# Kernel tuning notes

Hardware: AMD Instinct MI355X
Metric: run time of the kernel (lower is better)

Reference implementation:

```python
import jax, jax.numpy as jnp
import numpy as np

DATA_DIM = 8
NOISE_DIM = 8
HIDDEN = 128
N_STEPS = 100
BATCH = 65536


def _mlp3(tx, w1, b1, w2, b2, w3, b3):
    h = jnp.tanh(tx @ w1 + b1)
    h = jnp.tanh(h @ w2 + b2)
    return h @ w3 + b3


def setup_inputs() -> dict:
    key = jax.random.key(0)
    ks = jax.random.split(key, 20)
    s = 0.05
    d, nd, h = DATA_DIM, NOISE_DIM, HIDDEN
    inp = {
        "x": jax.random.normal(ks[0], (BATCH, d), jnp.float32),
        "initial_noise": jax.random.normal(ks[1], (BATCH, nd), jnp.float32),
        "dW": jax.random.normal(ks[2], (N_STEPS - 1, BATCH, nd), jnp.float32),
        # drift MLP: (1+d) -> h -> h -> d
        "drift_w1": jax.random.normal(ks[3], (1 + d, h), jnp.float32) * s,
        "drift_b1": jnp.zeros((h,), jnp.float32),
        "drift_w2": jax.random.normal(ks[4], (h, h), jnp.float32) * s,
        "drift_b2": jnp.zeros((h,), jnp.float32),
        "drift_w3": jax.random.normal(ks[5], (h, d), jnp.float32) * s,
        "drift_b3": jnp.zeros((d,), jnp.float32),
        # diffusion MLP: (1+d) -> h -> h -> d*nd
        "diff_w1": jax.random.normal(ks[6], (1 + d, h), jnp.float32) * s,
        "diff_b1": jnp.zeros((h,), jnp.float32),
        "diff_w2": jax.random.normal(ks[7], (h, h), jnp.float32) * s,
        "diff_b2": jnp.zeros((h,), jnp.float32),
        "diff_w3": jax.random.normal(ks[8], (h, d * nd), jnp.float32) * s,
        "diff_b3": jnp.zeros((d * nd,), jnp.float32),
        # initial-condition MLP: nd -> h -> d (num_layers=2)
        "init_w1": jax.random.normal(ks[9], (nd, h), jnp.float32) * s,
        "init_b1": jnp.zeros((h,), jnp.float32),
        "init_w2": jax.random.normal(ks[10], (h, d), jnp.float32) * s,
        "init_b2": jnp.zeros((d,), jnp.float32),
    }
    return inp


def reference(x, initial_noise, dW,
              drift_w1, drift_b1, drift_w2, drift_b2, drift_w3, drift_b3,
              diff_w1, diff_b1, diff_w2, diff_b2, diff_w3, diff_b3,
              init_w1, init_b1, init_w2, init_b2):
    batch = x.shape[0]
    n_steps = dW.shape[0] + 1
    dt = 1.0 / (n_steps - 1)
    sqrt_dt = jnp.sqrt(jnp.float32(dt))
    t_span = jnp.linspace(0.0, 1.0, n_steps, dtype=x.dtype)

    # initial condition: initial_net(noise)
    x0 = jnp.tanh(initial_noise @ init_w1 + init_b1) @ init_w2 + init_b2  # [B, d]

    def step(xc, inputs):
        t, dWi = inputs  # t scalar, dWi [B, nd]
        tcol = jnp.full((batch, 1), t, dtype=xc.dtype)
        tx = jnp.concatenate([tcol, xc], axis=1)  # [B, 1+d]
        f = _mlp3(tx, drift_w1, drift_b1, drift_w2, drift_b2, drift_w3, drift_b3)  # [B, d]
        g = _mlp3(tx, diff_w1, diff_b1, diff_w2, diff_b2, diff_w3, diff_b3)
        g = g.reshape(batch, DATA_DIM, NOISE_DIM)  # [B, d, nd]
        # Euler-Maruyama update: dx = f*dt + g @ (dW*sqrt(dt))
        dx = f * dt + jnp.einsum('bdn,bn->bd', g, dWi * sqrt_dt)
        xn = xc + dx
        return xn, xn

    _, xs = jax.lax.scan(step, x0, (t_span[:-1], dW))  # xs: [T-1, B, d]
    path = jnp.concatenate([x0[None], xs], axis=0)  # [T, B, d]
    path = jnp.transpose(path, (1, 0, 2))  # [B, T, d]
    return path.reshape(batch, -1)  # data_dim > 1 branch of forward
```

## Files before the change

### kernel.cpp

```cpp
#include <hip/hip_runtime.h>

typedef short bf16x8 __attribute__((ext_vector_type(8)));
typedef float f32x16 __attribute__((ext_vector_type(16)));
typedef unsigned int u32;
typedef unsigned int u32x4 __attribute__((ext_vector_type(4)));

#define NB 65536
#define STR2 136
#define STR1 24
#define OFF_W1  0
#define OFF_W2D 6144
#define OFF_W2F 23552
#define OFF_W3D 40960
#define OFF_W3F 45312
#define LDS_SHORTS 54016

__device__ __forceinline__ u32 bfr(float f) {
    u32 u = __builtin_bit_cast(u32, f);
    return (u + 0x7fffu + ((u >> 16) & 1u)) >> 16;
}
__device__ __forceinline__ u32 pkbf16(float a, float b) {
    return bfr(a) | (bfr(b) << 16);
}
__device__ __forceinline__ short bf16s(float a) {
    return (short)bfr(a);
}
__device__ __forceinline__ float ftanh(float x) {
    float e = __expf(2.0f * x);
    float r = __builtin_amdgcn_rcpf(e + 1.0f);
    return __builtin_fmaf(-2.0f, r, 1.0f);
}
__device__ __forceinline__ bf16x8 fragU(u32 a, u32 b, u32 c, u32 d) {
    u32x4 q = {a, b, c, d};
    return __builtin_bit_cast(bf16x8, q);
}
__device__ __forceinline__ bf16x8 fragV(u32x4 q) {
    return __builtin_bit_cast(bf16x8, q);
}
__device__ __forceinline__ bf16x8 ldsfrag(const short* p) {
    const u32x4* q = (const u32x4*)p;
    return __builtin_bit_cast(bf16x8, *q);
}
__device__ __forceinline__ f32x16 mf(bf16x8 a, bf16x8 b, f32x16 c) {
    return __builtin_amdgcn_mfma_f32_32x32x16_bf16(a, b, c, 0, 0, 0);
}

struct F2 { u32x4 a, b; };
__device__ __forceinline__ F2 transition(const f32x16 d, int hi) {
    u32 P[8], Q[8];
    #pragma unroll
    for (int i = 0; i < 8; ++i)
        P[i] = pkbf16(ftanh(d[2*i]), ftanh(d[2*i+1]));
    #pragma unroll
    for (int i = 0; i < 8; ++i)
        Q[i] = __shfl_xor(P[i], 32, 64);
    F2 r;
    r.a[0] = hi ? Q[2] : P[0];   r.a[1] = hi ? Q[3] : P[1];
    r.a[2] = hi ? P[2] : Q[0];   r.a[3] = hi ? P[3] : Q[1];
    r.b[0] = hi ? Q[6] : P[4];   r.b[1] = hi ? Q[7] : P[5];
    r.b[2] = hi ? P[6] : Q[4];   r.b[3] = hi ? P[7] : Q[5];
    return r;
}

__global__ __launch_bounds__(512, 2)
void sde_fused(const float* __restrict__ noise, const float* __restrict__ dW,
               const float* __restrict__ dw1, const float* __restrict__ db1,
               const float* __restrict__ dw2, const float* __restrict__ db2,
               const float* __restrict__ dw3, const float* __restrict__ db3,
               const float* __restrict__ fw1, const float* __restrict__ fb1,
               const float* __restrict__ fw2, const float* __restrict__ fb2,
               const float* __restrict__ fw3, const float* __restrict__ fb3,
               const float* __restrict__ iw1, const float* __restrict__ ib1,
               const float* __restrict__ iw2, const float* __restrict__ ib2,
               float* __restrict__ out)
{
    extern __shared__ short lds[];
    const int tid  = threadIdx.x;
    const int lane = tid & 63;
    const int col  = lane & 31;
    const int hi   = lane >> 5;
    const int wid  = tid >> 6;
    const int row  = blockIdx.x * 256 + wid * 32 + col;

    for (int idx = tid; idx < LDS_SHORTS; idx += 512) lds[idx] = 0;
    __syncthreads();
    for (int idx = tid; idx < 128*128; idx += 512) {
        int k = idx >> 7, m = idx & 127;
        lds[OFF_W2D + m*STR2 + k] = bf16s(dw2[idx]);
        lds[OFF_W2F + m*STR2 + k] = bf16s(fw2[idx]);
    }
    for (int idx = tid; idx < 128*64; idx += 512) {
        int k = idx >> 6, m = idx & 63;
        lds[OFF_W3F + m*STR2 + k] = bf16s(fw3[idx]);
    }
    for (int idx = tid; idx < 128*8; idx += 512) {
        int k = idx >> 3, m = idx & 7;
        lds[OFF_W3D + m*STR2 + k] = bf16s(dw3[idx]);
    }
    for (int idx = tid; idx < 9*128; idx += 512) {
        int k = idx >> 7, m = idx & 127;
        lds[OFF_W1 + m*STR1 + k]       = bf16s(dw1[idx]);
        lds[OFF_W1 + (m+128)*STR1 + k] = bf16s(fw1[idx]);
    }
    if (tid < 128) {
        lds[OFF_W1 + tid*STR1 + 9]       = bf16s(db1[tid]);
        lds[OFF_W1 + (tid+128)*STR1 + 9] = bf16s(fb1[tid]);
    }

    const bf16x8 BB = fragU(hi ? 0u : 0x3F80u, 0u, 0u, 0u);

    float x[8];
    {
        const float4 n0 = *(const float4*)(noise + (size_t)row*8);
        const float4 n1 = *(const float4*)(noise + (size_t)row*8 + 4);
        bf16x8 Bi = fragU(hi ? pkbf16(1.f,0.f) : pkbf16(n0.x,n0.y),
                          hi ? 0u : pkbf16(n0.z,n0.w),
                          hi ? 0u : pkbf16(n1.x,n1.y),
                          hi ? 0u : pkbf16(n1.z,n1.w));
        u32x4 Hf[8];
        #pragma unroll
        for (int mt = 0; mt < 4; ++mt) {
            int m = mt*32 + col;
            float wv[8];
            #pragma unroll
            for (int j = 0; j < 8; ++j) {
                int k = hi*8 + j;
                float v = 0.f;
                if (k < 8) v = iw1[(size_t)k*128 + m];
                else if (k == 8) v = ib1[m];
                wv[j] = v;
            }
            bf16x8 A = fragU(pkbf16(wv[0],wv[1]), pkbf16(wv[2],wv[3]),
                             pkbf16(wv[4],wv[5]), pkbf16(wv[6],wv[7]));
            f32x16 dacc = {};
            dacc = mf(A, Bi, dacc);
            F2 t = transition(dacc, hi);
            Hf[2*mt] = t.a; Hf[2*mt+1] = t.b;
        }
        f32x16 dx0 = {};
        #pragma unroll
        for (int kt = 0; kt < 8; ++kt) {
            float wv[8];
            #pragma unroll
            for (int j = 0; j < 8; ++j) {
                int k = kt*16 + hi*8 + j;
                wv[j] = (col < 8) ? iw2[(size_t)k*8 + col] : 0.f;
            }
            bf16x8 A = fragU(pkbf16(wv[0],wv[1]), pkbf16(wv[2],wv[3]),
                             pkbf16(wv[4],wv[5]), pkbf16(wv[6],wv[7]));
            dx0 = mf(A, fragV(Hf[kt]), dx0);
        }
        u32 ba = (!hi && col < 8) ? pkbf16(ib2[col], 0.f) : 0u;
        dx0 = mf(fragU(ba,0u,0u,0u), BB, dx0);
        #pragma unroll
        for (int r = 0; r < 4; ++r) {
            float cv  = dx0[r];
            float clo = hi ? 0.f : cv;
            float chi = hi ? cv  : 0.f;
            x[r]   = clo + __shfl_xor(clo, 32, 64);
            x[r+4] = chi + __shfl_xor(chi, 32, 64);
        }
    }

    u32 ba2d[4], ba2f[4], ba3f[2], ba3d;
    #pragma unroll
    for (int mt = 0; mt < 4; ++mt) {
        ba2d[mt] = hi ? 0u : pkbf16(db2[mt*32+col], 0.f);
        ba2f[mt] = hi ? 0u : pkbf16(fb2[mt*32+col], 0.f);
    }
    ba3f[0] = hi ? 0u : pkbf16(fb3[col], 0.f);
    ba3f[1] = hi ? 0u : pkbf16(fb3[32+col], 0.f);
    ba3d    = (!hi && col < 8) ? pkbf16(db3[col], 0.f) : 0u;

    __syncthreads();

    const short* pW1  = lds + OFF_W1  + col*STR1 + hi*8;
    const short* pW2d = lds + OFF_W2D + col*STR2 + hi*8;
    const short* pW2f = lds + OFF_W2F + col*STR2 + hi*8;
    const short* pW3d = lds + OFF_W3D + col*STR2 + hi*8;
    const short* pW3f = lds + OFF_W3F + col*STR2 + hi*8;

    const float dtv  = 1.0f / 99.0f;
    const float sqdt = sqrtf(dtv);
    const float* dwp = dW + (size_t)row*8 + hi*4;
    float* outr = out + (size_t)row*800;

    float xp[8];
    #pragma unroll
    for (int d = 0; d < 8; ++d) xp[d] = x[d];

    #pragma unroll 1
    for (int st = 0; st < 99; ++st) {
        const float tv = (float)st * dtv;
        const float4 dv = *(const float4*)(dwp + (size_t)st * (NB*8));

        u32 c0 = hi ? pkbf16(x[7], 1.0f) : pkbf16(tv, x[0]);
        u32 c1 = hi ? 0u : pkbf16(x[1], x[2]);
        u32 c2 = hi ? 0u : pkbf16(x[3], x[4]);
        u32 c3 = hi ? 0u : pkbf16(x[5], x[6]);
        bf16x8 B1 = fragU(c0, c1, c2, c3);

        u32x4 B2[8], B3[8];
        #pragma unroll
        for (int mt = 0; mt < 4; ++mt) {
            f32x16 dacc = {};
            dacc = mf(ldsfrag(pW1 + mt*32*STR1), B1, dacc);
            F2 t = transition(dacc, hi);
            B2[2*mt] = t.a; B2[2*mt+1] = t.b;
        }
        #pragma unroll
        for (int mt = 0; mt < 4; ++mt) {
            f32x16 dacc = {};
            #pragma unroll
            for (int kt = 0; kt < 8; ++kt)
                dacc = mf(ldsfrag(pW2d + mt*32*STR2 + kt*16), fragV(B2[kt]), dacc);
            dacc = mf(fragU(ba2d[mt],0u,0u,0u), BB, dacc);
            F2 t = transition(dacc, hi);
            B3[2*mt] = t.a; B3[2*mt+1] = t.b;
        }
        f32x16 fa = {};
        #pragma unroll
        for (int kt = 0; kt < 8; ++kt)
            fa = mf(ldsfrag(pW3d + kt*16), fragV(B3[kt]), fa);
        fa = mf(fragU(ba3d,0u,0u,0u), BB, fa);
        const float f0 = fa[0], f1 = fa[1], f2 = fa[2], f3 = fa[3];

        #pragma unroll
        for (int mt = 0; mt < 4; ++mt) {
            f32x16 dacc = {};
            dacc = mf(ldsfrag(pW1 + (mt+4)*32*STR1), B1, dacc);
            F2 t = transition(dacc, hi);
            B2[2*mt] = t.a; B2[2*mt+1] = t.b;
        }
        #pragma unroll
        for (int mt = 0; mt < 4; ++mt) {
            f32x16 dacc = {};
            #pragma unroll
            for (int kt = 0; kt < 8; ++kt)
                dacc = mf(ldsfrag(pW2f + mt*32*STR2 + kt*16), fragV(B2[kt]), dacc);
            dacc = mf(fragU(ba2f[mt],0u,0u,0u), BB, dacc);
            F2 t = transition(dacc, hi);
            B3[2*mt] = t.a; B3[2*mt+1] = t.b;
        }

        float p[8] = {0.f,0.f,0.f,0.f,0.f,0.f,0.f,0.f};
        const float dws[4] = {dv.x*sqdt, dv.y*sqdt, dv.z*sqdt, dv.w*sqdt};
        #pragma unroll
        for (int gt = 0; gt < 2; ++gt) {
            f32x16 g = {};
            #pragma unroll
            for (int kt = 0; kt < 8; ++kt)
                g = mf(ldsfrag(pW3f + gt*32*STR2 + kt*16), fragV(B3[kt]), g);
            g = mf(fragU(ba3f[gt],0u,0u,0u), BB, g);
            #pragma unroll
            for (int r = 0; r < 16; ++r)
                p[gt*4 + (r>>2)] += g[r] * dws[r&3];
        }

        #pragma unroll
        for (int r = 0; r < 4; ++r) {
            float fv = (r==0?f0:r==1?f1:r==2?f2:f3) * dtv;
            p[r]   += hi ? 0.f : fv;
            p[r+4] += hi ? fv  : 0.f;
        }
        #pragma unroll
        for (int d = 0; d < 8; ++d)
            x[d] += p[d] + __shfl_xor(p[d], 32, 64);

        if ((st & 1) == 0) {
            const float* src = hi ? x : xp;
            float4 o0, o1;
            o0.x = src[0]; o0.y = src[1]; o0.z = src[2]; o0.w = src[3];
            o1.x = src[4]; o1.y = src[5]; o1.z = src[6]; o1.w = src[7];
            float* dst = outr + (size_t)(st + hi) * 8;
            *(float4*)dst       = o0;
            *(float4*)(dst + 4) = o1;
        } else {
            #pragma unroll
            for (int d = 0; d < 8; ++d) xp[d] = x[d];
        }
    }
}

extern "C" void kernel_launch(void* const* d_in, const int* in_sizes, int n_in,
                              void* d_out, int out_size, void* d_ws, size_t ws_size,
                              hipStream_t stream) {
    const float* noise = (const float*)d_in[1];
    const float* dW    = (const float*)d_in[2];
    const float* dw1   = (const float*)d_in[3];
    const float* db1   = (const float*)d_in[4];
    const float* dw2   = (const float*)d_in[5];
    const float* db2   = (const float*)d_in[6];
    const float* dw3   = (const float*)d_in[7];
    const float* db3   = (const float*)d_in[8];
    const float* fw1   = (const float*)d_in[9];
    const float* fb1   = (const float*)d_in[10];
    const float* fw2   = (const float*)d_in[11];
    const float* fb2   = (const float*)d_in[12];
    const float* fw3   = (const float*)d_in[13];
    const float* fb3   = (const float*)d_in[14];
    const float* iw1   = (const float*)d_in[15];
    const float* ib1   = (const float*)d_in[16];
    const float* iw2   = (const float*)d_in[17];
    const float* ib2   = (const float*)d_in[18];
    float* out = (float*)d_out;
    sde_fused<<<dim3(256), dim3(512), LDS_SHORTS*sizeof(short), stream>>>(
        noise, dW, dw1, db1, dw2, db2, dw3, db3,
        fw1, fb1, fw2, fb2, fw3, fb3, iw1, ib1, iw2, ib2, out);
}
```

Baseline: 3.373 ms.

## Permute weight K layout to remove cross-lane shuffles in MFMA layer transitions

Reorders the K dimension of every weight matrix stored in LDS (and of the init-net weights and first-layer input packing) with a fixed bit permutation. The MFMA accumulator output of one layer can then be fed directly as the B operand of the next layer without the 8 xor-32 shuffles and selects per tile. This removes many DPP/permute ops in the hot 99-step loop. The launch bound is also re-expressed via amdgpu_waves_per_eu(2,2), which may change register allocation. Correctness depends on the permutation matching the MFMA register layout exactly.

```diff
diff --git a/kernel.cpp b/kernel.cpp
--- a/kernel.cpp
+++ b/kernel.cpp
@@ -15,6 +15,10 @@
 #define OFF_W3F 45312
 #define LDS_SHORTS 54016
 
+__device__ __host__ __forceinline__ int kappa(int v) {
+    return (v & 3) | ((v & 4) << 1) | ((v & 8) >> 1);
+}
+
 __device__ __forceinline__ u32 bfr(float f) {
     u32 u = __builtin_bit_cast(u32, f);
     return (u + 0x7fffu + ((u >> 16) & 1u)) >> 16;
@@ -46,23 +50,21 @@
 }
 
 struct F2 { u32x4 a, b; };
-__device__ __forceinline__ F2 transition(const f32x16 d, int hi) {
-    u32 P[8], Q[8];
-    #pragma unroll
-    for (int i = 0; i < 8; ++i)
-        P[i] = pkbf16(ftanh(d[2*i]), ftanh(d[2*i+1]));
-    #pragma unroll
-    for (int i = 0; i < 8; ++i)
-        Q[i] = __shfl_xor(P[i], 32, 64);
+__device__ __forceinline__ F2 transition(const f32x16 d) {
     F2 r;
-    r.a[0] = hi ? Q[2] : P[0];   r.a[1] = hi ? Q[3] : P[1];
-    r.a[2] = hi ? P[2] : Q[0];   r.a[3] = hi ? P[3] : Q[1];
-    r.b[0] = hi ? Q[6] : P[4];   r.b[1] = hi ? Q[7] : P[5];
-    r.b[2] = hi ? P[6] : Q[4];   r.b[3] = hi ? P[7] : Q[5];
+    r.a[0] = pkbf16(ftanh(d[0]),  ftanh(d[1]));
+    r.a[1] = pkbf16(ftanh(d[2]),  ftanh(d[3]));
+    r.a[2] = pkbf16(ftanh(d[4]),  ftanh(d[5]));
+    r.a[3] = pkbf16(ftanh(d[6]),  ftanh(d[7]));
+    r.b[0] = pkbf16(ftanh(d[8]),  ftanh(d[9]));
+    r.b[1] = pkbf16(ftanh(d[10]), ftanh(d[11]));
+    r.b[2] = pkbf16(ftanh(d[12]), ftanh(d[13]));
+    r.b[3] = pkbf16(ftanh(d[14]), ftanh(d[15]));
     return r;
 }
 
-__global__ __launch_bounds__(512, 2)
+__attribute__((amdgpu_waves_per_eu(2, 2)))
+__global__ __launch_bounds__(512)
 void sde_fused(const float* __restrict__ noise, const float* __restrict__ dW,
                const float* __restrict__ dw1, const float* __restrict__ db1,
                const float* __restrict__ dw2, const float* __restrict__ db2,
@@ -86,25 +88,29 @@
     __syncthreads();
     for (int idx = tid; idx < 128*128; idx += 512) {
         int k = idx >> 7, m = idx & 127;
-        lds[OFF_W2D + m*STR2 + k] = bf16s(dw2[idx]);
-        lds[OFF_W2F + m*STR2 + k] = bf16s(fw2[idx]);
+        int pos = (k & ~15) | kappa(k & 15);
+        lds[OFF_W2D + m*STR2 + pos] = bf16s(dw2[idx]);
+        lds[OFF_W2F + m*STR2 + pos] = bf16s(fw2[idx]);
     }
     for (int idx = tid; idx < 128*64; idx += 512) {
         int k = idx >> 6, m = idx & 63;
-        lds[OFF_W3F + m*STR2 + k] = bf16s(fw3[idx]);
+        int pos = (k & ~15) | kappa(k & 15);
+        lds[OFF_W3F + m*STR2 + pos] = bf16s(fw3[idx]);
     }
     for (int idx = tid; idx < 128*8; idx += 512) {
         int k = idx >> 3, m = idx & 7;
-        lds[OFF_W3D + m*STR2 + k] = bf16s(dw3[idx]);
+        int pos = (k & ~15) | kappa(k & 15);
+        lds[OFF_W3D + m*STR2 + pos] = bf16s(dw3[idx]);
     }
     for (int idx = tid; idx < 9*128; idx += 512) {
         int k = idx >> 7, m = idx & 127;
-        lds[OFF_W1 + m*STR1 + k]       = bf16s(dw1[idx]);
-        lds[OFF_W1 + (m+128)*STR1 + k] = bf16s(fw1[idx]);
+        int pos = kappa(k);
+        lds[OFF_W1 + m*STR1 + pos]       = bf16s(dw1[idx]);
+        lds[OFF_W1 + (m+128)*STR1 + pos] = bf16s(fw1[idx]);
     }
     if (tid < 128) {
-        lds[OFF_W1 + tid*STR1 + 9]       = bf16s(db1[tid]);
-        lds[OFF_W1 + (tid+128)*STR1 + 9] = bf16s(fb1[tid]);
+        lds[OFF_W1 + tid*STR1 + 5]       = bf16s(db1[tid]);
+        lds[OFF_W1 + (tid+128)*STR1 + 5] = bf16s(fb1[tid]);
     }
 
     const bf16x8 BB = fragU(hi ? 0u : 0x3F80u, 0u, 0u, 0u);
@@ -113,10 +119,10 @@
     {
         const float4 n0 = *(const float4*)(noise + (size_t)row*8);
         const float4 n1 = *(const float4*)(noise + (size_t)row*8 + 4);
-        bf16x8 Bi = fragU(hi ? pkbf16(1.f,0.f) : pkbf16(n0.x,n0.y),
-                          hi ? 0u : pkbf16(n0.z,n0.w),
-                          hi ? 0u : pkbf16(n1.x,n1.y),
-                          hi ? 0u : pkbf16(n1.z,n1.w));
+        bf16x8 Bi = fragU(hi ? pkbf16(n1.x,n1.y) : pkbf16(n0.x,n0.y),
+                          hi ? pkbf16(n1.z,n1.w) : pkbf16(n0.z,n0.w),
+                          hi ? 0u : pkbf16(1.f,0.f),
+                          0u);
         u32x4 Hf[8];
         #pragma unroll
         for (int mt = 0; mt < 4; ++mt) {
@@ -124,7 +130,7 @@
             float wv[8];
             #pragma unroll
             for (int j = 0; j < 8; ++j) {
-                int k = hi*8 + j;
+                int k = kappa(hi*8 + j);
                 float v = 0.f;
                 if (k < 8) v = iw1[(size_t)k*128 + m];
                 else if (k == 8) v = ib1[m];
@@ -134,7 +140,7 @@
                              pkbf16(wv[4],wv[5]), pkbf16(wv[6],wv[7]));
             f32x16 dacc = {};
             dacc = mf(A, Bi, dacc);
-            F2 t = transition(dacc, hi);
+            F2 t = transition(dacc);
             Hf[2*mt] = t.a; Hf[2*mt+1] = t.b;
         }
         f32x16 dx0 = {};
@@ -143,7 +149,7 @@
             float wv[8];
             #pragma unroll
             for (int j = 0; j < 8; ++j) {
-                int k = kt*16 + hi*8 + j;
+                int k = kt*16 + kappa(hi*8 + j);
                 wv[j] = (col < 8) ? iw2[(size_t)k*8 + col] : 0.f;
             }
             bf16x8 A = fragU(pkbf16(wv[0],wv[1]), pkbf16(wv[2],wv[3]),
@@ -194,18 +200,17 @@
         const float tv = (float)st * dtv;
         const float4 dv = *(const float4*)(dwp + (size_t)st * (NB*8));
 
-        u32 c0 = hi ? pkbf16(x[7], 1.0f) : pkbf16(tv, x[0]);
-        u32 c1 = hi ? 0u : pkbf16(x[1], x[2]);
-        u32 c2 = hi ? 0u : pkbf16(x[3], x[4]);
-        u32 c3 = hi ? 0u : pkbf16(x[5], x[6]);
-        bf16x8 B1 = fragU(c0, c1, c2, c3);
+        u32 c0 = hi ? pkbf16(x[3], x[4]) : pkbf16(tv, x[0]);
+        u32 c1 = hi ? pkbf16(x[5], x[6]) : pkbf16(x[1], x[2]);
+        u32 c2 = hi ? 0u : pkbf16(x[7], 1.0f);
+        bf16x8 B1 = fragU(c0, c1, c2, 0u);
 
         u32x4 B2[8], B3[8];
         #pragma unroll
         for (int mt = 0; mt < 4; ++mt) {
             f32x16 dacc = {};
             dacc = mf(ldsfrag(pW1 + mt*32*STR1), B1, dacc);
-            F2 t = transition(dacc, hi);
+            F2 t = transition(dacc);
             B2[2*mt] = t.a; B2[2*mt+1] = t.b;
         }
         #pragma unroll
@@ -215,7 +220,7 @@
             for (int kt = 0; kt < 8; ++kt)
                 dacc = mf(ldsfrag(pW2d + mt*32*STR2 + kt*16), fragV(B2[kt]), dacc);
             dacc = mf(fragU(ba2d[mt],0u,0u,0u), BB, dacc);
-            F2 t = transition(dacc, hi);
+            F2 t = transition(dacc);
             B3[2*mt] = t.a; B3[2*mt+1] = t.b;
         }
         f32x16 fa = {};
@@ -229,7 +234,7 @@
         for (int mt = 0; mt < 4; ++mt) {
             f32x16 dacc = {};
             dacc = mf(ldsfrag(pW1 + (mt+4)*32*STR1), B1, dacc);
-            F2 t = transition(dacc, hi);
+            F2 t = transition(dacc);
             B2[2*mt] = t.a; B2[2*mt+1] = t.b;
         }
         #pragma unroll
@@ -239,7 +244,7 @@
             for (int kt = 0; kt < 8; ++kt)
                 dacc = mf(ldsfrag(pW2f + mt*32*STR2 + kt*16), fragV(B2[kt]), dacc);
             dacc = mf(fragU(ba2f[mt],0u,0u,0u), BB, dacc);
-            F2 t = transition(dacc, hi);
+            F2 t = transition(dacc);
             B3[2*mt] = t.a; B3[2*mt+1] = t.b;
         }
 
```

Result: faster. 3.300 ms (-2.2%).
